# Optimization experiments

Hardware: AMD Instinct MI355X
Metric: run time of the kernel (lower is better)

The kernel has to match this reference:

```python
import jax, jax.numpy as jnp
import numpy as np

B, T, HID = 64, 2048, 512
H_CLS, D_OUT = 1024, 10


def setup_inputs() -> dict:
    key = jax.random.key(0)
    ks = jax.random.split(key, 9)
    std = 0.05
    return {
        "numerical": jax.random.normal(ks[0], (B, 16), dtype=jnp.float32),
        "embedding": jax.random.normal(ks[1], (B, T, HID), dtype=jnp.float32),
        "weight": jax.random.normal(ks[2], (HID, HID), dtype=jnp.float32) * std,
        "bias": jax.random.normal(ks[3], (1, HID), dtype=jnp.float32) * std,
        "context_weight": jax.random.normal(ks[4], (HID, 1), dtype=jnp.float32) * std,
        "W1": jax.random.normal(ks[5], (HID, H_CLS), dtype=jnp.float32) * 0.02,
        "b1": jnp.zeros((H_CLS,), dtype=jnp.float32),
        "W2": jax.random.normal(ks[6], (H_CLS, D_OUT), dtype=jnp.float32) * 0.02,
        "b2": jnp.zeros((D_OUT,), dtype=jnp.float32),
    }


def reference(numerical, embedding, weight, bias, context_weight, W1, b1, W2, b2):
    # matrix_mul(embedding.permute(1,0,2), weight, bias): per-timestep mm+bias+tanh
    # fused into one batched op. embedding: [B, T, HID]
    u = jnp.tanh(jnp.einsum('bth,hk->btk', embedding, weight) + bias)  # [B,T,HID]
    # matrix_mul(u, context_weight): mm + tanh, squeeze last dim -> [B,T]
    scores = jnp.tanh(jnp.einsum('bth,ho->bto', u, context_weight))[..., 0]  # [B,T]
    attn = jax.nn.softmax(scores, axis=1)  # softmax over time
    # element_wise_mul: weighted sum over time -> [B, HID]
    ctx = jnp.einsum('bth,bt->bh', embedding, attn)
    # classifier: Linear -> ReLU -> Linear -> Softmax(dim=1)
    h = jax.nn.relu(ctx @ W1 + b1)
    logits = h @ W2 + b2
    return jax.nn.softmax(logits, axis=1)
```

## Files before the change

### kernel.cpp

```cpp
#include <hip/hip_runtime.h>
#include <hip/hip_bf16.h>

typedef unsigned short u16;
typedef __attribute__((ext_vector_type(4))) float f32x4;
typedef __attribute__((ext_vector_type(8))) short bf16x8;
typedef __attribute__((ext_vector_type(8))) unsigned short u16x8;
typedef __attribute__((ext_vector_type(4))) unsigned short u16x4;

#define B_    64
#define T_    2048
#define HID_  512
#define HCLS_ 1024
#define DOUT_ 10
#define M_    (B_ * T_)

__device__ __forceinline__ unsigned f2bf2(float a, float b) {
#if __has_builtin(__builtin_amdgcn_cvt_pk_bf16_f32)
  auto r = __builtin_amdgcn_cvt_pk_bf16_f32(a, b);
  unsigned u;
  __builtin_memcpy(&u, &r, 4);
  return u;
#else
  unsigned ua = __float_as_uint(a) + 0x8000u;
  unsigned ub = __float_as_uint(b) + 0x8000u;
  return __builtin_amdgcn_perm(ub, ua, 0x07060302);
#endif
}

__device__ __forceinline__ float fast_tanh(float x) {
  float e = __expf(2.0f * x);
  return 1.0f - __fdividef(2.0f, e + 1.0f);
}

__global__ __launch_bounds__(256) void cvt_w_kernel(const float* __restrict__ W,
                                                    u16* __restrict__ Wt2) {
  const int pair = blockIdx.x * 4 + (threadIdx.x >> 6);
  const int l = threadIdx.x & 63;
  const int jt = pair >> 4, ks = pair & 15;
  const int n = jt * 16 + (l & 15);
  const int k0 = ks * 32 + (l >> 4) * 8;
  union { unsigned u[4]; u16x8 v; } r;
#pragma unroll
  for (int j = 0; j < 4; ++j)
    r.u[j] = f2bf2(W[(size_t)(k0 + 2 * j) * HID_ + n],
                   W[(size_t)(k0 + 2 * j + 1) * HID_ + n]);
  *(u16x8*)(Wt2 + (size_t)pair * 512 + l * 8) = r.v;
}

__global__ __launch_bounds__(512, 4) void gemm_fused_kernel(
    const float* __restrict__ E, const u16* __restrict__ Wt2,
    const float* __restrict__ bias, const float* __restrict__ cw,
    float* __restrict__ num, float* __restrict__ den) {
  __shared__ u16 lA[64 * 512];
  __shared__ float red[8 * 64];
  __shared__ float earr[64];

  const int tid = threadIdx.x;
  const int m0 = blockIdx.x * 64;
  const int b = blockIdx.x >> 5;
  const int w = tid >> 6, l = tid & 63;
  const int lm = l & 15, lg = l >> 4;

  {
    const float* ag = E + (size_t)m0 * HID_ + tid * 4;
    float4 r[16];
#pragma unroll
    for (int s = 0; s < 16; ++s)
      r[s] = *(const float4*)(ag + (size_t)s * 2048);
#pragma unroll
    for (int s = 0; s < 16; ++s) {
      const int row = s * 4 + (tid >> 7);
      const int c = (tid & 127) >> 1;
      const int phys = c ^ (row & 7);
      union { unsigned u[2]; u16x4 v; } t;
      t.u[0] = f2bf2(r[s].x, r[s].y);
      t.u[1] = f2bf2(r[s].z, r[s].w);
      *(u16x4*)(lA + row * 512 + phys * 8 + (tid & 1) * 4) = t.v;
    }
  }

  const u16* bbase = Wt2 + (size_t)w * 32768 + (size_t)l * 8;
  bf16x8 bv0[4], bv1[4];
#pragma unroll
  for (int j = 0; j < 4; ++j) bv0[j] = *(const bf16x8*)(bbase + j * 8192);
#pragma unroll
  for (int j = 0; j < 4; ++j) bv1[j] = *(const bf16x8*)(bbase + j * 8192 + 512);

  __syncthreads();

  f32x4 acc[4][4] = {};
#pragma unroll 1
  for (int ks = 0; ks < 16; ks += 2) {
    {
      const u16* abase = lA + lm * 512 + (((ks * 4 + lg) ^ (lm & 7)) * 8);
#pragma unroll
      for (int i = 0; i < 4; ++i) {
        bf16x8 af = *(const bf16x8*)(abase + i * 16 * 512);
#pragma unroll
        for (int j = 0; j < 4; ++j)
          acc[i][j] = __builtin_amdgcn_mfma_f32_16x16x32_bf16(af, bv0[j], acc[i][j], 0, 0, 0);
      }
      if (ks + 2 < 16) {
#pragma unroll
        for (int j = 0; j < 4; ++j)
          bv0[j] = *(const bf16x8*)(bbase + j * 8192 + (size_t)(ks + 2) * 512);
      }
    }
    {
      const u16* abase = lA + lm * 512 + ((((ks + 1) * 4 + lg) ^ (lm & 7)) * 8);
#pragma unroll
      for (int i = 0; i < 4; ++i) {
        bf16x8 af = *(const bf16x8*)(abase + i * 16 * 512);
#pragma unroll
        for (int j = 0; j < 4; ++j)
          acc[i][j] = __builtin_amdgcn_mfma_f32_16x16x32_bf16(af, bv1[j], acc[i][j], 0, 0, 0);
      }
      if (ks + 3 < 16) {
#pragma unroll
        for (int j = 0; j < 4; ++j)
          bv1[j] = *(const bf16x8*)(bbase + j * 8192 + (size_t)(ks + 3) * 512);
      }
    }
  }

  float bj[4], cj[4];
#pragma unroll
  for (int j = 0; j < 4; ++j) {
    int n = w * 64 + j * 16 + lm;
    bj[j] = bias[n];
    cj[j] = cw[n];
  }
#pragma unroll
  for (int i = 0; i < 4; ++i) {
#pragma unroll
    for (int r = 0; r < 4; ++r) {
      float s = 0.f;
#pragma unroll
      for (int j = 0; j < 4; ++j)
        s = fmaf(fast_tanh(acc[i][j][r] + bj[j]), cj[j], s);
      s += __shfl_xor(s, 1, 64);
      s += __shfl_xor(s, 2, 64);
      s += __shfl_xor(s, 4, 64);
      s += __shfl_xor(s, 8, 64);
      if (lm == 0) red[w * 64 + i * 16 + lg * 4 + r] = s;
    }
  }
  __syncthreads();
  if (tid < 64) {
    float d = 0.f;
#pragma unroll
    for (int ww = 0; ww < 8; ++ww) d += red[ww * 64 + tid];
    float e = __expf(fast_tanh(d));
    earr[tid] = e;
    float se = e;
    se += __shfl_xor(se, 1, 64);
    se += __shfl_xor(se, 2, 64);
    se += __shfl_xor(se, 4, 64);
    se += __shfl_xor(se, 8, 64);
    se += __shfl_xor(se, 16, 64);
    se += __shfl_xor(se, 32, 64);
    if (tid == 0) atomicAdd(den + b, se);
  }
  __syncthreads();
  {
    const int c8 = tid >> 3, rb = tid & 7;
    const u16* nbase = lA + rb * 512 + ((c8 ^ rb) * 8);
    float a8[8] = {};
#pragma unroll
    for (int k = 0; k < 8; ++k) {
      int r = rb + 8 * k;
      float e = earr[r];
      u16x8 v = *(const u16x8*)(nbase + k * 8 * 512);
#pragma unroll
      for (int j = 0; j < 8; ++j)
        a8[j] = fmaf(e, __uint_as_float((unsigned)v[j] << 16), a8[j]);
    }
#pragma unroll
    for (int j = 0; j < 8; ++j) {
      a8[j] += __shfl_xor(a8[j], 1, 64);
      a8[j] += __shfl_xor(a8[j], 2, 64);
      a8[j] += __shfl_xor(a8[j], 4, 64);
    }
    if (rb == 0) {
#pragma unroll
      for (int j = 0; j < 8; ++j)
        atomicAdd(num + (size_t)b * HID_ + c8 * 8 + j, a8[j]);
    }
  }
}

__global__ __launch_bounds__(1024) void classifier_kernel(
    const float* __restrict__ num, const float* __restrict__ den,
    const float* __restrict__ W1, const float* __restrict__ b1,
    const float* __restrict__ W2, const float* __restrict__ b2,
    float* __restrict__ out) {
  __shared__ float sc[HID_];
  __shared__ float hbuf[HCLS_];
  __shared__ float lgs[DOUT_];
  int b = blockIdx.x, tid = threadIdx.x;
  if (tid < HID_) sc[tid] = num[(size_t)b * HID_ + tid] / den[b];
  __syncthreads();
  float a = b1[tid];
#pragma unroll 8
  for (int k = 0; k < HID_; ++k) a = fmaf(sc[k], W1[(size_t)k * HCLS_ + tid], a);
  hbuf[tid] = fmaxf(a, 0.f);
  __syncthreads();
  if (tid < 160) {
    int j = tid >> 4, p = tid & 15;
    float acc2 = 0.f;
    for (int k = p; k < HCLS_; k += 16) acc2 = fmaf(hbuf[k], W2[(size_t)k * DOUT_ + j], acc2);
    acc2 += __shfl_xor(acc2, 1, 64);
    acc2 += __shfl_xor(acc2, 2, 64);
    acc2 += __shfl_xor(acc2, 4, 64);
    acc2 += __shfl_xor(acc2, 8, 64);
    if (p == 0) lgs[j] = acc2 + b2[j];
  }
  __syncthreads();
  if (tid == 0) {
    float mx = lgs[0];
#pragma unroll
    for (int j = 1; j < DOUT_; ++j) mx = fmaxf(mx, lgs[j]);
    float ex[DOUT_], s = 0.f;
#pragma unroll
    for (int j = 0; j < DOUT_; ++j) { ex[j] = __expf(lgs[j] - mx); s += ex[j]; }
    float inv = 1.f / s;
#pragma unroll
    for (int j = 0; j < DOUT_; ++j) out[b * DOUT_ + j] = ex[j] * inv;
  }
}

extern "C" void kernel_launch(void* const* d_in, const int* in_sizes, int n_in,
                              void* d_out, int out_size, void* d_ws, size_t ws_size,
                              hipStream_t stream) {
  (void)in_sizes; (void)n_in; (void)out_size; (void)ws_size;
  const float* E    = (const float*)d_in[1];
  const float* W    = (const float*)d_in[2];
  const float* bias = (const float*)d_in[3];
  const float* cw   = (const float*)d_in[4];
  const float* W1   = (const float*)d_in[5];
  const float* b1   = (const float*)d_in[6];
  const float* W2   = (const float*)d_in[7];
  const float* b2   = (const float*)d_in[8];
  float* out = (float*)d_out;

  u16*   Wt2 = (u16*)d_ws;
  float* num = (float*)((char*)d_ws + (512 << 10));
  float* den = (float*)((char*)d_ws + (512 << 10) + B_ * HID_ * sizeof(float));

  hipMemsetAsync(num, 0, (B_ * HID_ + B_) * sizeof(float), stream);
  cvt_w_kernel<<<128, 256, 0, stream>>>(W, Wt2);
  gemm_fused_kernel<<<M_ / 64, 512, 0, stream>>>(E, Wt2, bias, cw, num, den);
  classifier_kernel<<<B_, 1024, 0, stream>>>(num, den, W1, b1, W2, b2, out);
}
```

Measured before the change: 503.8 us.

## Double tile rows and stream embedding K-chunks into LDS during MFMA loop

Each block now handles 128 rows instead of 64. The embedding tile is loaded in 64-column chunks that are prefetched into registers and written to LDS while MFMAs run on the previous chunk, instead of a single upfront load. This targets load latency in the prologue and improves reuse of the weight fragments, but it doubles LDS use and accumulator registers, lowering occupancy and adding a barrier per chunk. The classifier loops also get larger unroll factors.

```diff
diff --git a/kernel.cpp b/kernel.cpp
--- a/kernel.cpp
+++ b/kernel.cpp
@@ -47,79 +47,100 @@
   *(u16x8*)(Wt2 + (size_t)pair * 512 + l * 8) = r.v;
 }
 
-__global__ __launch_bounds__(512, 4) void gemm_fused_kernel(
+__global__ __launch_bounds__(512, 2) void gemm_fused_kernel(
     const float* __restrict__ E, const u16* __restrict__ Wt2,
     const float* __restrict__ bias, const float* __restrict__ cw,
     float* __restrict__ num, float* __restrict__ den) {
-  __shared__ u16 lA[64 * 512];
-  __shared__ float red[8 * 64];
-  __shared__ float earr[64];
+  __shared__ u16 lA[128 * 512];
+  __shared__ float red[8 * 128];
+  __shared__ float earr[128];
 
   const int tid = threadIdx.x;
-  const int m0 = blockIdx.x * 64;
-  const int b = blockIdx.x >> 5;
+  const int m0 = blockIdx.x * 128;
+  const int b = blockIdx.x >> 4;
   const int w = tid >> 6, l = tid & 63;
   const int lm = l & 15, lg = l >> 4;
 
+  const int col4 = tid & 15;
+  const int row0 = tid >> 4;
+  const float* eb = E + (size_t)(m0 + row0) * HID_ + col4 * 4;
+
   {
-    const float* ag = E + (size_t)m0 * HID_ + tid * 4;
-    float4 r[16];
-#pragma unroll
-    for (int s = 0; s < 16; ++s)
-      r[s] = *(const float4*)(ag + (size_t)s * 2048);
-#pragma unroll
-    for (int s = 0; s < 16; ++s) {
-      const int row = s * 4 + (tid >> 7);
-      const int c = (tid & 127) >> 1;
-      const int phys = c ^ (row & 7);
+    float4 rg[4];
+#pragma unroll
+    for (int s = 0; s < 4; ++s) rg[s] = *(const float4*)(eb + (size_t)s * 32 * HID_);
+#pragma unroll
+    for (int s = 0; s < 4; ++s) {
+      const int r = row0 + s * 32;
+      const int phys = (col4 >> 1) ^ (r & 7);
       union { unsigned u[2]; u16x4 v; } t;
-      t.u[0] = f2bf2(r[s].x, r[s].y);
-      t.u[1] = f2bf2(r[s].z, r[s].w);
-      *(u16x4*)(lA + row * 512 + phys * 8 + (tid & 1) * 4) = t.v;
+      t.u[0] = f2bf2(rg[s].x, rg[s].y);
+      t.u[1] = f2bf2(rg[s].z, rg[s].w);
+      *(u16x4*)(lA + r * 512 + phys * 8 + (col4 & 1) * 4) = t.v;
     }
   }
 
   const u16* bbase = Wt2 + (size_t)w * 32768 + (size_t)l * 8;
-  bf16x8 bv0[4], bv1[4];
-#pragma unroll
-  for (int j = 0; j < 4; ++j) bv0[j] = *(const bf16x8*)(bbase + j * 8192);
-#pragma unroll
-  for (int j = 0; j < 4; ++j) bv1[j] = *(const bf16x8*)(bbase + j * 8192 + 512);
-
-  __syncthreads();
-
-  f32x4 acc[4][4] = {};
+  bf16x8 bvA[4], bvB[4];
+#pragma unroll
+  for (int j = 0; j < 4; ++j) bvA[j] = *(const bf16x8*)(bbase + j * 8192);
+#pragma unroll
+  for (int j = 0; j < 4; ++j) bvB[j] = *(const bf16x8*)(bbase + j * 8192 + 512);
+
+  __syncthreads();
+
+  f32x4 acc[8][4] = {};
 #pragma unroll 1
-  for (int ks = 0; ks < 16; ks += 2) {
+  for (int c = 0; c < 8; ++c) {
+    float4 rg[4];
+    if (c < 7) {
+#pragma unroll
+      for (int s = 0; s < 4; ++s)
+        rg[s] = *(const float4*)(eb + (c + 1) * 64 + (size_t)s * 32 * HID_);
+    }
     {
-      const u16* abase = lA + lm * 512 + (((ks * 4 + lg) ^ (lm & 7)) * 8);
-#pragma unroll
-      for (int i = 0; i < 4; ++i) {
+      const int ks0 = 2 * c;
+      const u16* abase = lA + lm * 512 + (((ks0 * 4 + lg) ^ (lm & 7)) * 8);
+#pragma unroll
+      for (int i = 0; i < 8; ++i) {
         bf16x8 af = *(const bf16x8*)(abase + i * 16 * 512);
 #pragma unroll
         for (int j = 0; j < 4; ++j)
-          acc[i][j] = __builtin_amdgcn_mfma_f32_16x16x32_bf16(af, bv0[j], acc[i][j], 0, 0, 0);
-      }
-      if (ks + 2 < 16) {
-#pragma unroll
-        for (int j = 0; j < 4; ++j)
-          bv0[j] = *(const bf16x8*)(bbase + j * 8192 + (size_t)(ks + 2) * 512);
+          acc[i][j] = __builtin_amdgcn_mfma_f32_16x16x32_bf16(af, bvA[j], acc[i][j], 0, 0, 0);
+      }
+      if (c < 7) {
+#pragma unroll
+        for (int j = 0; j < 4; ++j)
+          bvA[j] = *(const bf16x8*)(bbase + j * 8192 + (size_t)(ks0 + 2) * 512);
       }
     }
     {
-      const u16* abase = lA + lm * 512 + ((((ks + 1) * 4 + lg) ^ (lm & 7)) * 8);
-#pragma unroll
-      for (int i = 0; i < 4; ++i) {
+      const int ks1 = 2 * c + 1;
+      const u16* abase = lA + lm * 512 + (((ks1 * 4 + lg) ^ (lm & 7)) * 8);
+#pragma unroll
+      for (int i = 0; i < 8; ++i) {
         bf16x8 af = *(const bf16x8*)(abase + i * 16 * 512);
 #pragma unroll
         for (int j = 0; j < 4; ++j)
-          acc[i][j] = __builtin_amdgcn_mfma_f32_16x16x32_bf16(af, bv1[j], acc[i][j], 0, 0, 0);
-      }
-      if (ks + 3 < 16) {
-#pragma unroll
-        for (int j = 0; j < 4; ++j)
-          bv1[j] = *(const bf16x8*)(bbase + j * 8192 + (size_t)(ks + 3) * 512);
-      }
+          acc[i][j] = __builtin_amdgcn_mfma_f32_16x16x32_bf16(af, bvB[j], acc[i][j], 0, 0, 0);
+      }
+      if (c < 7) {
+#pragma unroll
+        for (int j = 0; j < 4; ++j)
+          bvB[j] = *(const bf16x8*)(bbase + j * 8192 + (size_t)(ks1 + 2) * 512);
+      }
+    }
+    if (c < 7) {
+#pragma unroll
+      for (int s = 0; s < 4; ++s) {
+        const int r = row0 + s * 32;
+        const int phys = ((c + 1) * 8 + (col4 >> 1)) ^ (r & 7);
+        union { unsigned u[2]; u16x4 v; } t;
+        t.u[0] = f2bf2(rg[s].x, rg[s].y);
+        t.u[1] = f2bf2(rg[s].z, rg[s].w);
+        *(u16x4*)(lA + r * 512 + phys * 8 + (col4 & 1) * 4) = t.v;
+      }
+      __syncthreads();
     }
   }
 
@@ -131,7 +152,7 @@
     cj[j] = cw[n];
   }
 #pragma unroll
-  for (int i = 0; i < 4; ++i) {
+  for (int i = 0; i < 8; ++i) {
 #pragma unroll
     for (int r = 0; r < 4; ++r) {
       float s = 0.f;
@@ -142,14 +163,14 @@
       s += __shfl_xor(s, 2, 64);
       s += __shfl_xor(s, 4, 64);
       s += __shfl_xor(s, 8, 64);
-      if (lm == 0) red[w * 64 + i * 16 + lg * 4 + r] = s;
-    }
-  }
-  __syncthreads();
-  if (tid < 64) {
+      if (lm == 0) red[w * 128 + i * 16 + lg * 4 + r] = s;
+    }
+  }
+  __syncthreads();
+  if (tid < 128) {
     float d = 0.f;
 #pragma unroll
-    for (int ww = 0; ww < 8; ++ww) d += red[ww * 64 + tid];
+    for (int ww = 0; ww < 8; ++ww) d += red[ww * 128 + tid];
     float e = __expf(fast_tanh(d));
     earr[tid] = e;
     float se = e;
@@ -159,7 +180,7 @@
     se += __shfl_xor(se, 8, 64);
     se += __shfl_xor(se, 16, 64);
     se += __shfl_xor(se, 32, 64);
-    if (tid == 0) atomicAdd(den + b, se);
+    if ((tid & 63) == 0) atomicAdd(den + b, se);
   }
   __syncthreads();
   {
@@ -167,7 +188,7 @@
     const u16* nbase = lA + rb * 512 + ((c8 ^ rb) * 8);
     float a8[8] = {};
 #pragma unroll
-    for (int k = 0; k < 8; ++k) {
+    for (int k = 0; k < 16; ++k) {
       int r = rb + 8 * k;
       float e = earr[r];
       u16x8 v = *(const u16x8*)(nbase + k * 8 * 512);
@@ -201,13 +222,14 @@
   if (tid < HID_) sc[tid] = num[(size_t)b * HID_ + tid] / den[b];
   __syncthreads();
   float a = b1[tid];
-#pragma unroll 8
+#pragma unroll 16
   for (int k = 0; k < HID_; ++k) a = fmaf(sc[k], W1[(size_t)k * HCLS_ + tid], a);
   hbuf[tid] = fmaxf(a, 0.f);
   __syncthreads();
   if (tid < 160) {
     int j = tid >> 4, p = tid & 15;
     float acc2 = 0.f;
+#pragma unroll 8
     for (int k = p; k < HCLS_; k += 16) acc2 = fmaf(hbuf[k], W2[(size_t)k * DOUT_ + j], acc2);
     acc2 += __shfl_xor(acc2, 1, 64);
     acc2 += __shfl_xor(acc2, 2, 64);
@@ -249,6 +271,6 @@
 
   hipMemsetAsync(num, 0, (B_ * HID_ + B_) * sizeof(float), stream);
   cvt_w_kernel<<<128, 256, 0, stream>>>(W, Wt2);
-  gemm_fused_kernel<<<M_ / 64, 512, 0, stream>>>(E, Wt2, bias, cw, num, den);
+  gemm_fused_kernel<<<M_ / 128, 512, 0, stream>>>(E, Wt2, bias, cw, num, den);
   classifier_kernel<<<B_, 1024, 0, stream>>>(num, den, W1, b1, W2, b2, out);
 }
```

Result: faster. 473.5 us (-6.0%).

## Stream embedding tiles directly into registers, dropping LDS staging in fused GEMM

Applied to the files above, without the earlier changes.

The fused GEMM no longer stages the 64x512 embedding tile in shared memory. Each lane loads fp32 embedding fragments straight from global memory, converts them to bf16 in registers and uses them as the B operand, while the weight fragments become the A operand, so the product is computed transposed. The weighted sum over time now rereads fp32 embedding from global memory or cache instead of the bf16 LDS copy. This drops 64KB of LDS per block and lowers the occupancy hint to 3, trading LDS traffic for more global or L2 reads, and the classifier loops get larger unroll factors.

```diff
diff --git a/kernel.cpp b/kernel.cpp
--- a/kernel.cpp
+++ b/kernel.cpp
@@ -5,7 +5,6 @@
 typedef __attribute__((ext_vector_type(4))) float f32x4;
 typedef __attribute__((ext_vector_type(8))) short bf16x8;
 typedef __attribute__((ext_vector_type(8))) unsigned short u16x8;
-typedef __attribute__((ext_vector_type(4))) unsigned short u16x4;
 
 #define B_    64
 #define T_    2048
@@ -47,11 +46,10 @@
   *(u16x8*)(Wt2 + (size_t)pair * 512 + l * 8) = r.v;
 }
 
-__global__ __launch_bounds__(512, 4) void gemm_fused_kernel(
+__global__ __launch_bounds__(512, 3) void gemm_fused_kernel(
     const float* __restrict__ E, const u16* __restrict__ Wt2,
     const float* __restrict__ bias, const float* __restrict__ cw,
     float* __restrict__ num, float* __restrict__ den) {
-  __shared__ u16 lA[64 * 512];
   __shared__ float red[8 * 64];
   __shared__ float earr[64];
 
@@ -61,89 +59,103 @@
   const int w = tid >> 6, l = tid & 63;
   const int lm = l & 15, lg = l >> 4;
 
-  {
-    const float* ag = E + (size_t)m0 * HID_ + tid * 4;
-    float4 r[16];
-#pragma unroll
-    for (int s = 0; s < 16; ++s)
-      r[s] = *(const float4*)(ag + (size_t)s * 2048);
-#pragma unroll
-    for (int s = 0; s < 16; ++s) {
-      const int row = s * 4 + (tid >> 7);
-      const int c = (tid & 127) >> 1;
-      const int phys = c ^ (row & 7);
-      union { unsigned u[2]; u16x4 v; } t;
-      t.u[0] = f2bf2(r[s].x, r[s].y);
-      t.u[1] = f2bf2(r[s].z, r[s].w);
-      *(u16x4*)(lA + row * 512 + phys * 8 + (tid & 1) * 4) = t.v;
-    }
-  }
-
-  const u16* bbase = Wt2 + (size_t)w * 32768 + (size_t)l * 8;
-  bf16x8 bv0[4], bv1[4];
-#pragma unroll
-  for (int j = 0; j < 4; ++j) bv0[j] = *(const bf16x8*)(bbase + j * 8192);
-#pragma unroll
-  for (int j = 0; j < 4; ++j) bv1[j] = *(const bf16x8*)(bbase + j * 8192 + 512);
-
-  __syncthreads();
+  const float* eb0 = E + (size_t)(m0 + lm) * HID_ + lg * 8;
+  const u16* abase = Wt2 + (size_t)w * 32768 + (size_t)l * 8;
 
   f32x4 acc[4][4] = {};
+  float4 er[4][2];
+  bf16x8 av0[4], av1[4];
+
+#pragma unroll
+  for (int j = 0; j < 4; ++j) {
+    er[j][0] = *(const float4*)(eb0 + (size_t)j * 16 * HID_);
+    er[j][1] = *(const float4*)(eb0 + (size_t)j * 16 * HID_ + 4);
+  }
+#pragma unroll
+  for (int i = 0; i < 4; ++i) av0[i] = *(const bf16x8*)(abase + i * 8192);
+#pragma unroll
+  for (int i = 0; i < 4; ++i) av1[i] = *(const bf16x8*)(abase + i * 8192 + 512);
+
 #pragma unroll 1
   for (int ks = 0; ks < 16; ks += 2) {
     {
-      const u16* abase = lA + lm * 512 + (((ks * 4 + lg) ^ (lm & 7)) * 8);
-#pragma unroll
-      for (int i = 0; i < 4; ++i) {
-        bf16x8 af = *(const bf16x8*)(abase + i * 16 * 512);
+      bf16x8 bf[4];
+#pragma unroll
+      for (int j = 0; j < 4; ++j) {
+        union { unsigned u[4]; bf16x8 v; } t;
+        t.u[0] = f2bf2(er[j][0].x, er[j][0].y);
+        t.u[1] = f2bf2(er[j][0].z, er[j][0].w);
+        t.u[2] = f2bf2(er[j][1].x, er[j][1].y);
+        t.u[3] = f2bf2(er[j][1].z, er[j][1].w);
+        bf[j] = t.v;
+      }
+#pragma unroll
+      for (int j = 0; j < 4; ++j) {
+        er[j][0] = *(const float4*)(eb0 + (size_t)j * 16 * HID_ + (ks + 1) * 32);
+        er[j][1] = *(const float4*)(eb0 + (size_t)j * 16 * HID_ + (ks + 1) * 32 + 4);
+      }
+#pragma unroll
+      for (int i = 0; i < 4; ++i)
 #pragma unroll
         for (int j = 0; j < 4; ++j)
-          acc[i][j] = __builtin_amdgcn_mfma_f32_16x16x32_bf16(af, bv0[j], acc[i][j], 0, 0, 0);
-      }
+          acc[i][j] = __builtin_amdgcn_mfma_f32_16x16x32_bf16(av0[i], bf[j], acc[i][j], 0, 0, 0);
       if (ks + 2 < 16) {
 #pragma unroll
-        for (int j = 0; j < 4; ++j)
-          bv0[j] = *(const bf16x8*)(bbase + j * 8192 + (size_t)(ks + 2) * 512);
+        for (int i = 0; i < 4; ++i)
+          av0[i] = *(const bf16x8*)(abase + i * 8192 + (size_t)(ks + 2) * 512);
       }
     }
     {
-      const u16* abase = lA + lm * 512 + ((((ks + 1) * 4 + lg) ^ (lm & 7)) * 8);
-#pragma unroll
-      for (int i = 0; i < 4; ++i) {
-        bf16x8 af = *(const bf16x8*)(abase + i * 16 * 512);
+      bf16x8 bf[4];
+#pragma unroll
+      for (int j = 0; j < 4; ++j) {
+        union { unsigned u[4]; bf16x8 v; } t;
+        t.u[0] = f2bf2(er[j][0].x, er[j][0].y);
+        t.u[1] = f2bf2(er[j][0].z, er[j][0].w);
+        t.u[2] = f2bf2(er[j][1].x, er[j][1].y);
+        t.u[3] = f2bf2(er[j][1].z, er[j][1].w);
+        bf[j] = t.v;
+      }
+      if (ks + 2 < 16) {
+#pragma unroll
+        for (int j = 0; j < 4; ++j) {
+          er[j][0] = *(const float4*)(eb0 + (size_t)j * 16 * HID_ + (ks + 2) * 32);
+          er[j][1] = *(const float4*)(eb0 + (size_t)j * 16 * HID_ + (ks + 2) * 32 + 4);
+        }
+      }
+#pragma unroll
+      for (int i = 0; i < 4; ++i)
 #pragma unroll
         for (int j = 0; j < 4; ++j)
-          acc[i][j] = __builtin_amdgcn_mfma_f32_16x16x32_bf16(af, bv1[j], acc[i][j], 0, 0, 0);
-      }
+          acc[i][j] = __builtin_amdgcn_mfma_f32_16x16x32_bf16(av1[i], bf[j], acc[i][j], 0, 0, 0);
       if (ks + 3 < 16) {
 #pragma unroll
-        for (int j = 0; j < 4; ++j)
-          bv1[j] = *(const bf16x8*)(bbase + j * 8192 + (size_t)(ks + 3) * 512);
+        for (int i = 0; i < 4; ++i)
+          av1[i] = *(const bf16x8*)(abase + i * 8192 + (size_t)(ks + 3) * 512);
       }
     }
   }
 
-  float bj[4], cj[4];
+  float s[4] = {0.f, 0.f, 0.f, 0.f};
+#pragma unroll
+  for (int i = 0; i < 4; ++i) {
+#pragma unroll
+    for (int r = 0; r < 4; ++r) {
+      const int n = w * 64 + i * 16 + lg * 4 + r;
+      const float bn = bias[n], cn = cw[n];
+#pragma unroll
+      for (int j = 0; j < 4; ++j)
+        s[j] = fmaf(fast_tanh(acc[i][j][r] + bn), cn, s[j]);
+    }
+  }
 #pragma unroll
   for (int j = 0; j < 4; ++j) {
-    int n = w * 64 + j * 16 + lm;
-    bj[j] = bias[n];
-    cj[j] = cw[n];
-  }
-#pragma unroll
-  for (int i = 0; i < 4; ++i) {
-#pragma unroll
-    for (int r = 0; r < 4; ++r) {
-      float s = 0.f;
-#pragma unroll
-      for (int j = 0; j < 4; ++j)
-        s = fmaf(fast_tanh(acc[i][j][r] + bj[j]), cj[j], s);
-      s += __shfl_xor(s, 1, 64);
-      s += __shfl_xor(s, 2, 64);
-      s += __shfl_xor(s, 4, 64);
-      s += __shfl_xor(s, 8, 64);
-      if (lm == 0) red[w * 64 + i * 16 + lg * 4 + r] = s;
-    }
+    s[j] += __shfl_xor(s[j], 16, 64);
+    s[j] += __shfl_xor(s[j], 32, 64);
+  }
+  if (lg == 0) {
+#pragma unroll
+    for (int j = 0; j < 4; ++j) red[w * 64 + j * 16 + lm] = s[j];
   }
   __syncthreads();
   if (tid < 64) {
@@ -163,29 +175,12 @@
   }
   __syncthreads();
   {
-    const int c8 = tid >> 3, rb = tid & 7;
-    const u16* nbase = lA + rb * 512 + ((c8 ^ rb) * 8);
-    float a8[8] = {};
-#pragma unroll
-    for (int k = 0; k < 8; ++k) {
-      int r = rb + 8 * k;
-      float e = earr[r];
-      u16x8 v = *(const u16x8*)(nbase + k * 8 * 512);
-#pragma unroll
-      for (int j = 0; j < 8; ++j)
-        a8[j] = fmaf(e, __uint_as_float((unsigned)v[j] << 16), a8[j]);
-    }
-#pragma unroll
-    for (int j = 0; j < 8; ++j) {
-      a8[j] += __shfl_xor(a8[j], 1, 64);
-      a8[j] += __shfl_xor(a8[j], 2, 64);
-      a8[j] += __shfl_xor(a8[j], 4, 64);
-    }
-    if (rb == 0) {
-#pragma unroll
-      for (int j = 0; j < 8; ++j)
-        atomicAdd(num + (size_t)b * HID_ + c8 * 8 + j, a8[j]);
-    }
+    float a = 0.f;
+    const float* ec = E + (size_t)m0 * HID_ + tid;
+#pragma unroll 8
+    for (int r = 0; r < 64; ++r)
+      a = fmaf(earr[r], ec[(size_t)r * HID_], a);
+    atomicAdd(num + (size_t)b * HID_ + tid, a);
   }
 }
 
@@ -201,13 +196,14 @@
   if (tid < HID_) sc[tid] = num[(size_t)b * HID_ + tid] / den[b];
   __syncthreads();
   float a = b1[tid];
-#pragma unroll 8
+#pragma unroll 16
   for (int k = 0; k < HID_; ++k) a = fmaf(sc[k], W1[(size_t)k * HCLS_ + tid], a);
   hbuf[tid] = fmaxf(a, 0.f);
   __syncthreads();
   if (tid < 160) {
     int j = tid >> 4, p = tid & 15;
     float acc2 = 0.f;
+#pragma unroll 8
     for (int k = p; k < HCLS_; k += 16) acc2 = fmaf(hbuf[k], W2[(size_t)k * DOUT_ + j], acc2);
     acc2 += __shfl_xor(acc2, 1, 64);
     acc2 += __shfl_xor(acc2, 2, 64);
```

Measured after the change: 705.7 us. +40.1%, slower.
